# Kernel tuning notes

Measured on AMD Instinct MI355X. Metric: run time of the kernel, lower is better.

## Reference

```python
import jax, jax.numpy as jnp
import numpy as np

N_NODES = 100000
N_EDGES = 1600000
IN_DIM, H1, H2, N_CLASSES = 128, 64, 64, 16
NEG_SLOPE = 0.2  # PyG GATConv default leaky_relu slope


def _xavier(key, shape, gain=1.414):
    fan_in, fan_out = shape[0], shape[-1]
    a = gain * np.sqrt(6.0 / (fan_in + fan_out))
    return jax.random.uniform(key, shape, jnp.float32, -a, a)


def setup_inputs() -> dict:
    key = jax.random.key(0)
    ks = jax.random.split(key, 12)
    ft_list = jax.random.normal(ks[0], (N_NODES, IN_DIM), jnp.float32)
    adj_tensor = jax.random.randint(ks[1], (2, N_EDGES), 0, N_NODES, jnp.int64)
    return {
        "ft_list": ft_list,
        "adj_tensor": adj_tensor,
        "W1": _xavier(ks[2], (IN_DIM, H1)),
        "a_src1": _xavier(ks[3], (H1, 1))[:, 0],
        "a_dst1": _xavier(ks[4], (H1, 1))[:, 0],
        "b1": jnp.zeros((H1,), jnp.float32),
        "W2": _xavier(ks[5], (H1, H2)),
        "a_src2": _xavier(ks[6], (H2, 1))[:, 0],
        "a_dst2": _xavier(ks[7], (H2, 1))[:, 0],
        "b2": jnp.zeros((H2,), jnp.float32),
        "clas_W": _xavier(ks[8], (H2, N_CLASSES)),
        "clas_b": _xavier(ks[9], (1, N_CLASSES)),
    }


def _gat_conv(x, src, dst, n, W, a_src, a_dst, b):
    # h: [N, H] transformed node features
    h = x @ W
    alpha_s = h @ a_src  # [N]
    alpha_d = h @ a_dst  # [N]
    # per-edge attention logit (gather)
    e = jax.nn.leaky_relu(alpha_s[src] + alpha_d[dst], NEG_SLOPE)  # [E]
    # segment softmax over edges grouped by destination node
    m = jax.ops.segment_max(e, dst, num_segments=n)
    p = jnp.exp(e - m[dst])
    s = jax.ops.segment_sum(p, dst, num_segments=n)
    attn = p / s[dst]  # [E]
    # weighted scatter-add of source features
    out = jax.ops.segment_sum(h[src] * attn[:, None], dst, num_segments=n)
    return out + b


def reference(ft_list, adj_tensor, W1, a_src1, a_dst1, b1, W2, a_src2, a_dst2, b2, clas_W, clas_b):
    n = ft_list.shape[0]
    loop = jnp.arange(n, dtype=adj_tensor.dtype)
    src = jnp.concatenate([adj_tensor[0], loop])  # add self-loops (PyG default)
    dst = jnp.concatenate([adj_tensor[1], loop])
    x = _gat_conv(ft_list, src, dst, n, W1, a_src1, a_dst1, b1)
    x = jax.nn.elu(x)
    # dropout(0.5) is identity in eval mode
    x = _gat_conv(x, src, dst, n, W2, a_src2, a_dst2, b2)
    logits = x @ clas_W + clas_b
    return logits, x
```

## Files before the change

### kernel.cpp

```cpp
#include <hip/hip_runtime.h>
#include <hip/hip_bf16.h>

#define NEG_SLOPE 0.2f
#define LOG2E 1.4426950408889634f
#define BSH 9
#define BW  (1 << BSH)
#define CH  4096
#define PGRID 256

typedef short short8 __attribute__((ext_vector_type(8)));
typedef float f32x4 __attribute__((ext_vector_type(4)));


__global__ __launch_bounds__(256) void bucket_hist_kernel(
    const int* __restrict__ adj, int* __restrict__ H, int E, int N, int R, int NBK)
{
    __shared__ int hist[256];
    const int t = threadIdx.x;
    const int ET = E + N;
    for (int r = blockIdx.x; r < R; r += gridDim.x) {
        hist[t] = 0;
        __syncthreads();
        int base = r * CH;
        for (int i = 0; i < CH / 256; ++i) {
            int e = base + i * 256 + t;
            if (e >= ET) break;
            int d = (e < E) ? adj[E + e] : (e - E);
            atomicAdd(&hist[d >> BSH], 1);
        }
        __syncthreads();
        if (t < NBK) H[r * NBK + t] = hist[t];
        __syncthreads();
    }
}

__global__ __launch_bounds__(256) void scan_rounds_kernel(
    const int* __restrict__ H, int* __restrict__ S2, int* __restrict__ tot,
    int R, int NBK)
{
    __shared__ int part[256];
    const int b = blockIdx.x;
    const int t = threadIdx.x;
    const int C = (R + 255) / 256;
    int r0 = t * C, r1 = min(R, r0 + C);
    int s = 0;
    for (int r = r0; r < r1; ++r) s += H[r * NBK + b];
    part[t] = s;
    __syncthreads();
    for (int off = 1; off < 256; off <<= 1) {
        int v = (t >= off) ? part[t - off] : 0;
        __syncthreads();
        part[t] += v;
        __syncthreads();
    }
    int run = (t > 0) ? part[t - 1] : 0;
    for (int r = r0; r < r1; ++r) {
        int h = H[r * NBK + b];
        S2[r * NBK + b] = run;
        run += h;
    }
    if (t == 255) tot[b] = part[255];
}

__global__ __launch_bounds__(256) void scan_tot_kernel(
    const int* __restrict__ tot, int* __restrict__ base, int NBK)
{
    __shared__ int s[256];
    int t = threadIdx.x;
    int v = (t < NBK) ? tot[t] : 0;
    s[t] = v;
    __syncthreads();
    for (int off = 1; off < 256; off <<= 1) {
        int u = (t >= off) ? s[t - off] : 0;
        __syncthreads();
        s[t] += u;
        __syncthreads();
    }
    if (t < NBK) base[t] = s[t] - v;
}

__global__ __launch_bounds__(256) void partition_kernel(
    const int* __restrict__ adj, const int* __restrict__ S2,
    const int* __restrict__ base, int* __restrict__ pbuf,
    int E, int N, int R, int NBK)
{
    __shared__ int lcur[256];
    const int t = threadIdx.x;
    const int ET = E + N;
    for (int r = blockIdx.x; r < R; r += gridDim.x) {
        if (t < NBK) lcur[t] = base[t] + S2[r * NBK + t];
        __syncthreads();
        int b0 = r * CH;
        for (int i = 0; i < CH / 256; ++i) {
            int e = b0 + i * 256 + t;
            if (e >= ET) break;
            int s, d;
            if (e < E) { d = adj[E + e]; s = adj[e]; }
            else       { s = d = e - E; }
            int b = d >> BSH;
            int pos = atomicAdd(&lcur[b], 1);
            pbuf[pos] = (s << BSH) | (d & (BW - 1));
        }
        __syncthreads();
    }
}

__global__ __launch_bounds__(256) void csr_build_kernel(
    const int* __restrict__ base, const int* __restrict__ tot,
    const int* __restrict__ pbuf,
    int* __restrict__ row_ptr, int* __restrict__ col_idx, int E, int N, int NBK)
{
    __shared__ int offA[BW];
    __shared__ int lcur[BW];
    const int b = blockIdx.x;
    const int t = threadIdx.x;
    const int node0 = b << BSH;
    const int nn = min(BW, N - node0);
    const int ET = E + N;
    const int segbeg = base[b];
    const int segend = segbeg + tot[b];

    offA[t] = 0; offA[t + 256] = 0;
    __syncthreads();
    for (int i = segbeg + t; i < segend; i += 256)
        atomicAdd(&offA[pbuf[i] & (BW - 1)], 1);
    __syncthreads();
    for (int off = 1; off < BW; off <<= 1) {
        int i1 = t + 256;
        int v0 = (t >= off) ? offA[t - off] : 0;
        int v1 = (i1 >= off) ? offA[i1 - off] : 0;
        __syncthreads();
        offA[t] += v0; offA[i1] += v1;
        __syncthreads();
    }
    if (t < nn) {
        int ex = t ? offA[t - 1] : 0;
        row_ptr[node0 + t] = segbeg + ex;
        lcur[t] = segbeg + ex;
    }
    int i2 = t + 256;
    if (i2 < nn) {
        int ex = offA[i2 - 1];
        row_ptr[node0 + i2] = segbeg + ex;
        lcur[i2] = segbeg + ex;
    }
    if (b == NBK - 1 && t == 0) row_ptr[N] = ET;
    __syncthreads();
    for (int i = segbeg + t; i < segend; i += 256) {
        int p = pbuf[i];
        int pos = atomicAdd(&lcur[p & (BW - 1)], 1);
        col_idx[pos] = p >> BSH;
    }
}


__device__ __forceinline__ unsigned short f2bf(float f)
{
    union { __hip_bfloat16 b; unsigned short u; } v;
    v.b = __float2bfloat16(f);
    return v.u;
}

__global__ __launch_bounds__(256) void prep_wfrag_kernel(
    const float* __restrict__ W, unsigned short* __restrict__ wf, int K)
{
    int total = K * 64;
    int idx = blockIdx.x * 256 + threadIdx.x;
    if (idx >= total) return;
    int i = idx & 7;
    int l = (idx >> 3) & 63;
    int f = idx >> 9;
    int s = f >> 2, tt = f & 3;
    int k = 32 * s + 8 * (l >> 4) + i;
    int n = 16 * tt + (l & 15);
    wf[idx] = f2bf(W[k * 64 + n]);
}

template<int K>
__global__ __launch_bounds__(256) void gemm_alpha_mfma(
    const float* __restrict__ X, const unsigned short* __restrict__ wf,
    const float* __restrict__ a_src, const float* __restrict__ a_dst,
    __hip_bfloat16* __restrict__ h, float* __restrict__ as_, float* __restrict__ ad_,
    int N, int nChunks)
{
    constexpr int S = K / 32;
    const int t = threadIdx.x;
    const int wave = t >> 6, lane = t & 63;
    const int g = lane >> 4, c = lane & 15;

    short8 bf[S * 4];
#pragma unroll
    for (int f = 0; f < S * 4; ++f)
        bf[f] = *(const short8*)(wf + ((size_t)(f * 64 + lane)) * 8);

    float asr[4], adr[4];
#pragma unroll
    for (int tt = 0; tt < 4; ++tt) {
        asr[tt] = a_src[16 * tt + c];
        adr[tt] = a_dst[16 * tt + c];
    }

    for (int chunk = blockIdx.x; chunk < nChunks; chunk += gridDim.x) {
        const int r0 = chunk * 64 + wave * 16;
        const int arow = r0 + c;
        const bool rv = arow < N;
        const float* xr = X + (size_t)arow * K;

        f32x4 acc[4];
#pragma unroll
        for (int tt = 0; tt < 4; ++tt) acc[tt] = (f32x4){0.f, 0.f, 0.f, 0.f};

#pragma unroll
        for (int s = 0; s < S; ++s) {
            float4 x0 = make_float4(0.f, 0.f, 0.f, 0.f);
            float4 x1 = make_float4(0.f, 0.f, 0.f, 0.f);
            if (rv) {
                const float4* p = (const float4*)(xr + 32 * s + 8 * g);
                x0 = p[0]; x1 = p[1];
            }
            float xs[8] = {x0.x, x0.y, x0.z, x0.w, x1.x, x1.y, x1.z, x1.w};
            union { short8 v; unsigned u[4]; } ah, al;
#pragma unroll
            for (int p2 = 0; p2 < 4; ++p2) {
                unsigned u0 = __float_as_uint(xs[2 * p2]);
                unsigned u1 = __float_as_uint(xs[2 * p2 + 1]);
                ah.u[p2] = (u0 >> 16) | (u1 & 0xffff0000u);
                float h0 = __uint_as_float(u0 & 0xffff0000u);
                float h1 = __uint_as_float(u1 & 0xffff0000u);
                unsigned l0 = __float_as_uint(xs[2 * p2] - h0);
                unsigned l1 = __float_as_uint(xs[2 * p2 + 1] - h1);
                al.u[p2] = (l0 >> 16) | (l1 & 0xffff0000u);
            }
#pragma unroll
            for (int tt = 0; tt < 4; ++tt) {
                acc[tt] = __builtin_amdgcn_mfma_f32_16x16x32_bf16(
                    ah.v, bf[s * 4 + tt], acc[tt], 0, 0, 0);
                acc[tt] = __builtin_amdgcn_mfma_f32_16x16x32_bf16(
                    al.v, bf[s * 4 + tt], acc[tt], 0, 0, 0);
            }
        }

#pragma unroll
        for (int i = 0; i < 4; ++i) {
            const int ri = r0 + 4 * g + i;
            float va = 0.f, vd = 0.f;
#pragma unroll
            for (int tt = 0; tt < 4; ++tt) {
                float v = acc[tt][i];
                va += v * asr[tt];
                vd += v * adr[tt];
                if (ri < N) h[(size_t)ri * 64 + 16 * tt + c] = __float2bfloat16(v);
            }
#pragma unroll
            for (int off = 8; off >= 1; off >>= 1) {
                va += __shfl_xor(va, off, 16);
                vd += __shfl_xor(vd, off, 16);
            }
            if (c == 0 && ri < N) { as_[ri] = va * LOG2E; ad_[ri] = vd * LOG2E; }
        }
    }
}

__global__ __launch_bounds__(256) void gat_aggregate_kernel(
    const int* __restrict__ row_ptr, const int* __restrict__ col_idx,
    const float* __restrict__ as_, const float* __restrict__ ad_,
    const __hip_bfloat16* __restrict__ h, const float* __restrict__ b,
    float* __restrict__ out, int N, int do_elu)
{
    const int wave = threadIdx.x >> 6, lane = threadIdx.x & 63;
    const int sub = lane >> 3, q = lane & 7;
    const int node = blockIdx.x * 32 + wave * 8 + sub;
    if (node >= N) return;
    const int beg = row_ptr[node], end = row_ptr[node + 1];
    const float ad = ad_[node];
    float acc[8] = {0.f, 0.f, 0.f, 0.f, 0.f, 0.f, 0.f, 0.f};
    float psum = 0.f;

    const char* cbp = (const char*)col_idx;
    const char* abp = (const char*)as_;
    const char* hbp = (const char*)h;
    const unsigned qb = (unsigned)q * 16u;

    unsigned co = (unsigned)beg * 4u;
    for (int i = beg; i < end; i += 2, co += 8u) {
        const bool v1 = (i + 1) < end;
        int s0 = *(const int*)(cbp + co);
        int s1 = *(const int*)(cbp + (v1 ? co + 4u : co));
        float x0 = *(const float*)(abp + ((unsigned)s0 << 2)) + ad;
        float x1 = *(const float*)(abp + ((unsigned)s1 << 2)) + ad;
        uint4 u0 = *(const uint4*)(hbp + (((unsigned)s0 << 7) + qb));
        uint4 u1 = *(const uint4*)(hbp + (((unsigned)s1 << 7) + qb));
        x0 = fmaxf(x0, NEG_SLOPE * x0);
        x1 = fmaxf(x1, NEG_SLOPE * x1);
        float p0 = __builtin_amdgcn_exp2f(x0);
        float p1 = v1 ? __builtin_amdgcn_exp2f(x1) : 0.f;
        psum += p0 + p1;
        unsigned w;
        w = u0.x; acc[0] += p0 * __uint_as_float(w << 16); acc[1] += p0 * __uint_as_float(w & 0xffff0000u);
        w = u0.y; acc[2] += p0 * __uint_as_float(w << 16); acc[3] += p0 * __uint_as_float(w & 0xffff0000u);
        w = u0.z; acc[4] += p0 * __uint_as_float(w << 16); acc[5] += p0 * __uint_as_float(w & 0xffff0000u);
        w = u0.w; acc[6] += p0 * __uint_as_float(w << 16); acc[7] += p0 * __uint_as_float(w & 0xffff0000u);
        w = u1.x; acc[0] += p1 * __uint_as_float(w << 16); acc[1] += p1 * __uint_as_float(w & 0xffff0000u);
        w = u1.y; acc[2] += p1 * __uint_as_float(w << 16); acc[3] += p1 * __uint_as_float(w & 0xffff0000u);
        w = u1.z; acc[4] += p1 * __uint_as_float(w << 16); acc[5] += p1 * __uint_as_float(w & 0xffff0000u);
        w = u1.w; acc[6] += p1 * __uint_as_float(w << 16); acc[7] += p1 * __uint_as_float(w & 0xffff0000u);
    }

    const float inv = 1.f / psum;
    const float* bq = b + q * 8;
    float4 b0 = *(const float4*)bq;
    float4 b1 = *(const float4*)(bq + 4);
    float v[8];
    v[0] = acc[0] * inv + b0.x; v[1] = acc[1] * inv + b0.y;
    v[2] = acc[2] * inv + b0.z; v[3] = acc[3] * inv + b0.w;
    v[4] = acc[4] * inv + b1.x; v[5] = acc[5] * inv + b1.y;
    v[6] = acc[6] * inv + b1.z; v[7] = acc[7] * inv + b1.w;
    if (do_elu) {
#pragma unroll
        for (int j = 0; j < 8; ++j)
            v[j] = v[j] > 0.f ? v[j] : (__expf(v[j]) - 1.f);
    }
    float* op = out + (size_t)node * 64 + q * 8;
    ((float4*)op)[0] = make_float4(v[0], v[1], v[2], v[3]);
    ((float4*)op)[1] = make_float4(v[4], v[5], v[6], v[7]);
}

__global__ __launch_bounds__(256) void classifier_kernel(
    const float* __restrict__ x, const float* __restrict__ cw,
    const float* __restrict__ cb, float* __restrict__ out, int N)
{
    int i = blockIdx.x * blockDim.x + threadIdx.x;
    if (i >= N * 16) return;
    int n = i >> 4, c = i & 15;
    const float4* xr = (const float4*)(x + (size_t)n * 64);
    float acc = cb[c];
#pragma unroll
    for (int j4 = 0; j4 < 16; ++j4) {
        float4 xv = xr[j4];
        acc += xv.x * cw[(j4 * 4 + 0) * 16 + c];
        acc += xv.y * cw[(j4 * 4 + 1) * 16 + c];
        acc += xv.z * cw[(j4 * 4 + 2) * 16 + c];
        acc += xv.w * cw[(j4 * 4 + 3) * 16 + c];
    }
    out[i] = acc;
}

extern "C" void kernel_launch(void* const* d_in, const int* in_sizes, int n_in,
                              void* d_out, int out_size, void* d_ws, size_t ws_size,
                              hipStream_t stream)
{
    const float* X    = (const float*)d_in[0];
    const int*   adj  = (const int*)d_in[1];
    const float* W1   = (const float*)d_in[2];
    const float* a_s1 = (const float*)d_in[3];
    const float* a_d1 = (const float*)d_in[4];
    const float* b1   = (const float*)d_in[5];
    const float* W2   = (const float*)d_in[6];
    const float* a_s2 = (const float*)d_in[7];
    const float* a_d2 = (const float*)d_in[8];
    const float* b2   = (const float*)d_in[9];
    const float* cW   = (const float*)d_in[10];
    const float* cb   = (const float*)d_in[11];

    const int N   = in_sizes[0] / 128;
    const int E   = in_sizes[1] / 2;
    const int ET  = E + N;
    const int R   = (ET + CH - 1) / CH;
    const int NBK = (N + BW - 1) >> BSH;

    __hip_bfloat16* A = (__hip_bfloat16*)d_ws;
    float* B       = (float*)(A + (size_t)N * 64);
    float* asb     = B + (size_t)N * 64;
    float* adb     = asb + N;
    int*   row_ptr = (int*)(adb + N);
    int*   col_idx = row_ptr + (N + 1);
    int*   pbuf    = col_idx + ET;
    int*   H       = pbuf + ET;
    int*   S2      = H + R * NBK;
    int*   tot     = S2 + R * NBK;
    int*   base    = tot + NBK;

    uintptr_t wp = ((uintptr_t)pbuf + 15) & ~(uintptr_t)15;
    unsigned short* wf1 = (unsigned short*)wp;
    unsigned short* wf2 = wf1 + 128 * 64;

    const int T = 256;
    const int aggBlocks  = (N + 31) / 32;
    const int nChunks    = (N + 63) / 64;
    const int gemmBlocks = nChunks < 512 ? nChunks : 512;

    bucket_hist_kernel<<<PGRID, T, 0, stream>>>(adj, H, E, N, R, NBK);
    scan_rounds_kernel<<<NBK, T, 0, stream>>>(H, S2, tot, R, NBK);
    scan_tot_kernel<<<1, T, 0, stream>>>(tot, base, NBK);
    partition_kernel<<<PGRID, T, 0, stream>>>(adj, S2, base, pbuf, E, N, R, NBK);
    csr_build_kernel<<<NBK, T, 0, stream>>>(base, tot, pbuf, row_ptr, col_idx, E, N, NBK);

    prep_wfrag_kernel<<<(128 * 64 + 255) / 256, T, 0, stream>>>(W1, wf1, 128);
    prep_wfrag_kernel<<<(64 * 64 + 255) / 256, T, 0, stream>>>(W2, wf2, 64);

    gemm_alpha_mfma<128><<<gemmBlocks, T, 0, stream>>>(
        X, wf1, a_s1, a_d1, A, asb, adb, N, nChunks);
    gat_aggregate_kernel<<<aggBlocks, T, 0, stream>>>(
        row_ptr, col_idx, asb, adb, A, b1, B, N, 1);

    float* out  = (float*)d_out;
    float* xout = out + (size_t)N * 16;
    gemm_alpha_mfma<64><<<gemmBlocks, T, 0, stream>>>(
        B, wf2, a_s2, a_d2, A, asb, adb, N, nChunks);
    gat_aggregate_kernel<<<aggBlocks, T, 0, stream>>>(
        row_ptr, col_idx, asb, adb, A, b2, xout, N, 0);

    classifier_kernel<<<(N * 16 + T - 1) / T, T, 0, stream>>>(
        xout, cW, cb, out, N);
}
```

Before: 299.6 us.

## Sort nodes by in-degree to balance aggregation work across wavefronts

Adds a counting sort of nodes by in-degree (histogram, scan, scatter) and has the aggregation kernels process nodes in that permuted order, so the 8 nodes sharing a wave have similar edge counts. This targets divergence and load imbalance, where a wave waits on its longest-degree node. It adds three small kernels plus an extra perm indirection, and it loses the locality of contiguous node order for outputs and row_ptr reads.

```diff
diff --git a/kernel.cpp b/kernel.cpp
--- a/kernel.cpp
+++ b/kernel.cpp
@@ -63,10 +63,12 @@
 }
 
 __global__ __launch_bounds__(256) void scan_tot_kernel(
-    const int* __restrict__ tot, int* __restrict__ base, int NBK)
+    const int* __restrict__ tot, int* __restrict__ base, int NBK,
+    int* __restrict__ gh)
 {
     __shared__ int s[256];
     int t = threadIdx.x;
+    gh[t] = 0;
     int v = (t < NBK) ? tot[t] : 0;
     s[t] = v;
     __syncthreads();
@@ -154,6 +156,58 @@
 }
 
 
+__global__ __launch_bounds__(256) void deg_hist_kernel(
+    const int* __restrict__ row_ptr, int* __restrict__ gh, int N)
+{
+    __shared__ int lh[256];
+    const int t = threadIdx.x;
+    lh[t] = 0;
+    __syncthreads();
+    for (int n = blockIdx.x * 256 + t; n < N; n += gridDim.x * 256)
+        atomicAdd(&lh[min(row_ptr[n + 1] - row_ptr[n], 255)], 1);
+    __syncthreads();
+    if (lh[t]) atomicAdd(&gh[t], lh[t]);
+}
+
+__global__ __launch_bounds__(256) void deg_scan_kernel(
+    const int* __restrict__ gh, int* __restrict__ gcur)
+{
+    __shared__ int s[256];
+    int t = threadIdx.x;
+    int v = gh[t];
+    s[t] = v;
+    __syncthreads();
+    for (int off = 1; off < 256; off <<= 1) {
+        int u = (t >= off) ? s[t - off] : 0;
+        __syncthreads();
+        s[t] += u;
+        __syncthreads();
+    }
+    gcur[t] = s[t] - v;
+}
+
+__global__ __launch_bounds__(256) void deg_scatter_kernel(
+    const int* __restrict__ row_ptr, int* __restrict__ gcur,
+    int* __restrict__ perm, int N)
+{
+    __shared__ int lh[256], lcur[256];
+    const int t = threadIdx.x;
+    const int n0 = blockIdx.x * 2048;
+    const int n1 = min(N, n0 + 2048);
+    lh[t] = 0;
+    __syncthreads();
+    for (int n = n0 + t; n < n1; n += 256)
+        atomicAdd(&lh[min(row_ptr[n + 1] - row_ptr[n], 255)], 1);
+    __syncthreads();
+    lcur[t] = lh[t] ? atomicAdd(&gcur[t], lh[t]) : 0;
+    __syncthreads();
+    for (int n = n0 + t; n < n1; n += 256) {
+        int pos = atomicAdd(&lcur[min(row_ptr[n + 1] - row_ptr[n], 255)], 1);
+        perm[pos] = n;
+    }
+}
+
+
 __device__ __forceinline__ unsigned short f2bf(float f)
 {
     union { __hip_bfloat16 b; unsigned short u; } v;
@@ -262,6 +316,7 @@
 }
 
 __global__ __launch_bounds__(256) void gat_aggregate_kernel(
+    const int* __restrict__ perm,
     const int* __restrict__ row_ptr, const int* __restrict__ col_idx,
     const float* __restrict__ as_, const float* __restrict__ ad_,
     const __hip_bfloat16* __restrict__ h, const float* __restrict__ b,
@@ -269,8 +324,9 @@
 {
     const int wave = threadIdx.x >> 6, lane = threadIdx.x & 63;
     const int sub = lane >> 3, q = lane & 7;
-    const int node = blockIdx.x * 32 + wave * 8 + sub;
-    if (node >= N) return;
+    const int idx = blockIdx.x * 32 + wave * 8 + sub;
+    if (idx >= N) return;
+    const int node = perm[idx];
     const int beg = row_ptr[node], end = row_ptr[node + 1];
     const float ad = ad_[node];
     float acc[8] = {0.f, 0.f, 0.f, 0.f, 0.f, 0.f, 0.f, 0.f};
@@ -379,6 +435,9 @@
     int*   S2      = H + R * NBK;
     int*   tot     = S2 + R * NBK;
     int*   base    = tot + NBK;
+    int*   perm    = base + NBK;
+    int*   gh      = perm + N;
+    int*   gcur    = gh + 256;
 
     uintptr_t wp = ((uintptr_t)pbuf + 15) & ~(uintptr_t)15;
     unsigned short* wf1 = (unsigned short*)wp;
@@ -391,9 +450,13 @@
 
     bucket_hist_kernel<<<PGRID, T, 0, stream>>>(adj, H, E, N, R, NBK);
     scan_rounds_kernel<<<NBK, T, 0, stream>>>(H, S2, tot, R, NBK);
-    scan_tot_kernel<<<1, T, 0, stream>>>(tot, base, NBK);
+    scan_tot_kernel<<<1, T, 0, stream>>>(tot, base, NBK, gh);
     partition_kernel<<<PGRID, T, 0, stream>>>(adj, S2, base, pbuf, E, N, R, NBK);
     csr_build_kernel<<<NBK, T, 0, stream>>>(base, tot, pbuf, row_ptr, col_idx, E, N, NBK);
+
+    deg_hist_kernel<<<128, T, 0, stream>>>(row_ptr, gh, N);
+    deg_scan_kernel<<<1, T, 0, stream>>>(gh, gcur);
+    deg_scatter_kernel<<<(N + 2047) / 2048, T, 0, stream>>>(row_ptr, gcur, perm, N);
 
     prep_wfrag_kernel<<<(128 * 64 + 255) / 256, T, 0, stream>>>(W1, wf1, 128);
     prep_wfrag_kernel<<<(64 * 64 + 255) / 256, T, 0, stream>>>(W2, wf2, 64);
@@ -401,14 +464,14 @@
     gemm_alpha_mfma<128><<<gemmBlocks, T, 0, stream>>>(
         X, wf1, a_s1, a_d1, A, asb, adb, N, nChunks);
     gat_aggregate_kernel<<<aggBlocks, T, 0, stream>>>(
-        row_ptr, col_idx, asb, adb, A, b1, B, N, 1);
+        perm, row_ptr, col_idx, asb, adb, A, b1, B, N, 1);
 
     float* out  = (float*)d_out;
     float* xout = out + (size_t)N * 16;
     gemm_alpha_mfma<64><<<gemmBlocks, T, 0, stream>>>(
         B, wf2, a_s2, a_d2, A, asb, adb, N, nChunks);
     gat_aggregate_kernel<<<aggBlocks, T, 0, stream>>>(
-        row_ptr, col_idx, asb, adb, A, b2, xout, N, 0);
+        perm, row_ptr, col_idx, asb, adb, A, b2, xout, N, 0);
 
     classifier_kernel<<<(N * 16 + T - 1) / T, T, 0, stream>>>(
         xout, cW, cb, out, N);
```

New measurement: 318.9 us. 1.06x slower.

## Fuse CSR construction into one persistent kernel with grid barriers; unroll aggregation by 8

Applied to the files above, without the earlier changes.

Replaces the five-kernel bucketed CSR build with a single persistent kernel that does a global-atomic degree count, a two-level scan, and an atomic scatter into col_idx, separated by software grid barriers. Weight fragment prep and counter zeroing are merged into one init kernel, cutting launch count. The aggregation loop now processes 8 edges per iteration so more gathers are in flight at once. In exchange it uses global atomics on 100k counters, which can contend, and it relies on all 256 blocks being co-resident for the barrier to avoid deadlock. The scatter also loses the bucketed locality the old partition step gave to col_idx writes.

```diff
diff --git a/kernel.cpp b/kernel.cpp
--- a/kernel.cpp
+++ b/kernel.cpp
@@ -3,156 +3,9 @@
 
 #define NEG_SLOPE 0.2f
 #define LOG2E 1.4426950408889634f
-#define BSH 9
-#define BW  (1 << BSH)
-#define CH  4096
-#define PGRID 256
 
 typedef short short8 __attribute__((ext_vector_type(8)));
 typedef float f32x4 __attribute__((ext_vector_type(4)));
-
-
-__global__ __launch_bounds__(256) void bucket_hist_kernel(
-    const int* __restrict__ adj, int* __restrict__ H, int E, int N, int R, int NBK)
-{
-    __shared__ int hist[256];
-    const int t = threadIdx.x;
-    const int ET = E + N;
-    for (int r = blockIdx.x; r < R; r += gridDim.x) {
-        hist[t] = 0;
-        __syncthreads();
-        int base = r * CH;
-        for (int i = 0; i < CH / 256; ++i) {
-            int e = base + i * 256 + t;
-            if (e >= ET) break;
-            int d = (e < E) ? adj[E + e] : (e - E);
-            atomicAdd(&hist[d >> BSH], 1);
-        }
-        __syncthreads();
-        if (t < NBK) H[r * NBK + t] = hist[t];
-        __syncthreads();
-    }
-}
-
-__global__ __launch_bounds__(256) void scan_rounds_kernel(
-    const int* __restrict__ H, int* __restrict__ S2, int* __restrict__ tot,
-    int R, int NBK)
-{
-    __shared__ int part[256];
-    const int b = blockIdx.x;
-    const int t = threadIdx.x;
-    const int C = (R + 255) / 256;
-    int r0 = t * C, r1 = min(R, r0 + C);
-    int s = 0;
-    for (int r = r0; r < r1; ++r) s += H[r * NBK + b];
-    part[t] = s;
-    __syncthreads();
-    for (int off = 1; off < 256; off <<= 1) {
-        int v = (t >= off) ? part[t - off] : 0;
-        __syncthreads();
-        part[t] += v;
-        __syncthreads();
-    }
-    int run = (t > 0) ? part[t - 1] : 0;
-    for (int r = r0; r < r1; ++r) {
-        int h = H[r * NBK + b];
-        S2[r * NBK + b] = run;
-        run += h;
-    }
-    if (t == 255) tot[b] = part[255];
-}
-
-__global__ __launch_bounds__(256) void scan_tot_kernel(
-    const int* __restrict__ tot, int* __restrict__ base, int NBK)
-{
-    __shared__ int s[256];
-    int t = threadIdx.x;
-    int v = (t < NBK) ? tot[t] : 0;
-    s[t] = v;
-    __syncthreads();
-    for (int off = 1; off < 256; off <<= 1) {
-        int u = (t >= off) ? s[t - off] : 0;
-        __syncthreads();
-        s[t] += u;
-        __syncthreads();
-    }
-    if (t < NBK) base[t] = s[t] - v;
-}
-
-__global__ __launch_bounds__(256) void partition_kernel(
-    const int* __restrict__ adj, const int* __restrict__ S2,
-    const int* __restrict__ base, int* __restrict__ pbuf,
-    int E, int N, int R, int NBK)
-{
-    __shared__ int lcur[256];
-    const int t = threadIdx.x;
-    const int ET = E + N;
-    for (int r = blockIdx.x; r < R; r += gridDim.x) {
-        if (t < NBK) lcur[t] = base[t] + S2[r * NBK + t];
-        __syncthreads();
-        int b0 = r * CH;
-        for (int i = 0; i < CH / 256; ++i) {
-            int e = b0 + i * 256 + t;
-            if (e >= ET) break;
-            int s, d;
-            if (e < E) { d = adj[E + e]; s = adj[e]; }
-            else       { s = d = e - E; }
-            int b = d >> BSH;
-            int pos = atomicAdd(&lcur[b], 1);
-            pbuf[pos] = (s << BSH) | (d & (BW - 1));
-        }
-        __syncthreads();
-    }
-}
-
-__global__ __launch_bounds__(256) void csr_build_kernel(
-    const int* __restrict__ base, const int* __restrict__ tot,
-    const int* __restrict__ pbuf,
-    int* __restrict__ row_ptr, int* __restrict__ col_idx, int E, int N, int NBK)
-{
-    __shared__ int offA[BW];
-    __shared__ int lcur[BW];
-    const int b = blockIdx.x;
-    const int t = threadIdx.x;
-    const int node0 = b << BSH;
-    const int nn = min(BW, N - node0);
-    const int ET = E + N;
-    const int segbeg = base[b];
-    const int segend = segbeg + tot[b];
-
-    offA[t] = 0; offA[t + 256] = 0;
-    __syncthreads();
-    for (int i = segbeg + t; i < segend; i += 256)
-        atomicAdd(&offA[pbuf[i] & (BW - 1)], 1);
-    __syncthreads();
-    for (int off = 1; off < BW; off <<= 1) {
-        int i1 = t + 256;
-        int v0 = (t >= off) ? offA[t - off] : 0;
-        int v1 = (i1 >= off) ? offA[i1 - off] : 0;
-        __syncthreads();
-        offA[t] += v0; offA[i1] += v1;
-        __syncthreads();
-    }
-    if (t < nn) {
-        int ex = t ? offA[t - 1] : 0;
-        row_ptr[node0 + t] = segbeg + ex;
-        lcur[t] = segbeg + ex;
-    }
-    int i2 = t + 256;
-    if (i2 < nn) {
-        int ex = offA[i2 - 1];
-        row_ptr[node0 + i2] = segbeg + ex;
-        lcur[i2] = segbeg + ex;
-    }
-    if (b == NBK - 1 && t == 0) row_ptr[N] = ET;
-    __syncthreads();
-    for (int i = segbeg + t; i < segend; i += 256) {
-        int p = pbuf[i];
-        int pos = atomicAdd(&lcur[p & (BW - 1)], 1);
-        col_idx[pos] = p >> BSH;
-    }
-}
-
 
 __device__ __forceinline__ unsigned short f2bf(float f)
 {
@@ -161,20 +14,118 @@
     return v.u;
 }
 
-__global__ __launch_bounds__(256) void prep_wfrag_kernel(
-    const float* __restrict__ W, unsigned short* __restrict__ wf, int K)
-{
-    int total = K * 64;
-    int idx = blockIdx.x * 256 + threadIdx.x;
-    if (idx >= total) return;
-    int i = idx & 7;
-    int l = (idx >> 3) & 63;
-    int f = idx >> 9;
-    int s = f >> 2, tt = f & 3;
-    int k = 32 * s + 8 * (l >> 4) + i;
-    int n = 16 * tt + (l & 15);
-    wf[idx] = f2bf(W[k * 64 + n]);
-}
+__global__ __launch_bounds__(256) void init_kernel(
+    const float* __restrict__ W1, const float* __restrict__ W2,
+    unsigned short* __restrict__ wf1, unsigned short* __restrict__ wf2,
+    int* __restrict__ cnt, int* __restrict__ bars, int N)
+{
+    const int tid = blockIdx.x * 256 + threadIdx.x;
+    if (tid < 16) bars[tid] = 0;
+    if (tid < 128 * 64) {
+        int i = tid & 7, l = (tid >> 3) & 63, f = tid >> 9;
+        int s = f >> 2, tt = f & 3;
+        wf1[tid] = f2bf(W1[(32 * s + 8 * (l >> 4) + i) * 64 + (16 * tt + (l & 15))]);
+    }
+    if (tid < 64 * 64) {
+        int i = tid & 7, l = (tid >> 3) & 63, f = tid >> 9;
+        int s = f >> 2, tt = f & 3;
+        wf2[tid] = f2bf(W2[(32 * s + 8 * (l >> 4) + i) * 64 + (16 * tt + (l & 15))]);
+    }
+    for (int n = tid; n < N; n += gridDim.x * 256) cnt[n] = 0;
+}
+
+__device__ __forceinline__ void grid_bar(int* bar, int nb)
+{
+    __syncthreads();
+    __threadfence();
+    if (threadIdx.x == 0) {
+        __hip_atomic_fetch_add(bar, 1, __ATOMIC_ACQ_REL, __HIP_MEMORY_SCOPE_AGENT);
+        while (__hip_atomic_load(bar, __ATOMIC_ACQUIRE, __HIP_MEMORY_SCOPE_AGENT) < nb)
+            __builtin_amdgcn_s_sleep(1);
+    }
+    __syncthreads();
+    __threadfence();
+}
+
+__global__ __launch_bounds__(256) void csr_fused_kernel(
+    const int* __restrict__ adj, int* __restrict__ cnt,
+    int* __restrict__ row_ptr, int* __restrict__ cur,
+    int* __restrict__ csum, int* __restrict__ bars,
+    int* __restrict__ col_idx, int E, int N)
+{
+    const int t = threadIdx.x;
+    const int b = blockIdx.x;
+    const int NB = gridDim.x;
+    const int ET = E + N;
+    const int gsz = NB * 256;
+    const int NC = (N + 255) >> 8;
+    __shared__ int s[512];
+
+    for (int i = b * 256 + t; i < ET; i += gsz) {
+        int d = (i < E) ? adj[E + i] : (i - E);
+        atomicAdd(&cnt[d], 1);
+    }
+    grid_bar(&bars[0], NB);
+
+    for (int c = b; c < NC; c += NB) {
+        int i = c * 256 + t;
+        int v = (i < N) ? cnt[i] : 0;
+        s[t] = v;
+        __syncthreads();
+        for (int off = 1; off < 256; off <<= 1) {
+            int u = (t >= off) ? s[t - off] : 0;
+            __syncthreads();
+            s[t] += u;
+            __syncthreads();
+        }
+        if (i < N) row_ptr[i] = s[t] - v;
+        if (t == 255)
+            __hip_atomic_store(&csum[c], s[255], __ATOMIC_RELEASE, __HIP_MEMORY_SCOPE_AGENT);
+        __syncthreads();
+    }
+    grid_bar(&bars[1], NB);
+
+    if (b == 0) {
+        int i1 = t + 256;
+        int v0 = (t < NC) ? __hip_atomic_load(&csum[t], __ATOMIC_ACQUIRE, __HIP_MEMORY_SCOPE_AGENT) : 0;
+        int v1 = (i1 < NC) ? __hip_atomic_load(&csum[i1], __ATOMIC_ACQUIRE, __HIP_MEMORY_SCOPE_AGENT) : 0;
+        s[t] = v0; s[i1] = v1;
+        __syncthreads();
+        for (int off = 1; off < 512; off <<= 1) {
+            int u0 = (t >= off) ? s[t - off] : 0;
+            int u1 = (i1 >= off) ? s[i1 - off] : 0;
+            __syncthreads();
+            s[t] += u0; s[i1] += u1;
+            __syncthreads();
+        }
+        int e0 = t ? s[t - 1] : 0;
+        int e1 = s[i1 - 1];
+        if (t < NC)  __hip_atomic_store(&csum[t],  e0, __ATOMIC_RELEASE, __HIP_MEMORY_SCOPE_AGENT);
+        if (i1 < NC) __hip_atomic_store(&csum[i1], e1, __ATOMIC_RELEASE, __HIP_MEMORY_SCOPE_AGENT);
+    }
+    grid_bar(&bars[2], NB);
+
+    for (int c = b; c < NC; c += NB) {
+        int off = __hip_atomic_load(&csum[c], __ATOMIC_ACQUIRE, __HIP_MEMORY_SCOPE_AGENT);
+        int i = c * 256 + t;
+        if (i < N) {
+            int rp = row_ptr[i] + off;
+            row_ptr[i] = rp;
+            __hip_atomic_store(&cur[i], rp, __ATOMIC_RELEASE, __HIP_MEMORY_SCOPE_AGENT);
+            if (i == N - 1) row_ptr[N] = rp + cnt[i];
+        }
+    }
+    grid_bar(&bars[3], NB);
+
+    for (int i = b * 256 + t; i < ET; i += gsz) {
+        int sn, d;
+        if (i < E) { sn = adj[i]; d = adj[E + i]; }
+        else       { sn = d = i - E; }
+        int pos = atomicAdd(&cur[d], 1);
+        col_idx[pos] = sn;
+    }
+}
+
 
 template<int K>
 __global__ __launch_bounds__(256) void gemm_alpha_mfma(
@@ -261,6 +212,12 @@
     }
 }
 
+#define ACC8(u, p)                                                              \
+    w = u.x; acc[0] += p * __uint_as_float(w << 16); acc[1] += p * __uint_as_float(w & 0xffff0000u); \
+    w = u.y; acc[2] += p * __uint_as_float(w << 16); acc[3] += p * __uint_as_float(w & 0xffff0000u); \
+    w = u.z; acc[4] += p * __uint_as_float(w << 16); acc[5] += p * __uint_as_float(w & 0xffff0000u); \
+    w = u.w; acc[6] += p * __uint_as_float(w << 16); acc[7] += p * __uint_as_float(w & 0xffff0000u);
+
 __global__ __launch_bounds__(256) void gat_aggregate_kernel(
     const int* __restrict__ row_ptr, const int* __restrict__ col_idx,
     const float* __restrict__ as_, const float* __restrict__ ad_,
@@ -280,30 +237,36 @@
     const char* abp = (const char*)as_;
     const char* hbp = (const char*)h;
     const unsigned qb = (unsigned)q * 16u;
-
+    unsigned w;
+
+    int i = beg;
     unsigned co = (unsigned)beg * 4u;
-    for (int i = beg; i < end; i += 2, co += 8u) {
-        const bool v1 = (i + 1) < end;
+    for (; i + 8 <= end; i += 8, co += 32u) {
+        int s[8];
+#pragma unroll
+        for (int k = 0; k < 8; ++k) s[k] = *(const int*)(cbp + (co + 4u * k));
+        float x[8];
+#pragma unroll
+        for (int k = 0; k < 8; ++k) x[k] = *(const float*)(abp + ((unsigned)s[k] << 2)) + ad;
+        uint4 u[8];
+#pragma unroll
+        for (int k = 0; k < 8; ++k) u[k] = *(const uint4*)(hbp + (((unsigned)s[k] << 7) + qb));
+#pragma unroll
+        for (int k = 0; k < 8; ++k) {
+            float xx = fmaxf(x[k], NEG_SLOPE * x[k]);
+            float p = __builtin_amdgcn_exp2f(xx);
+            psum += p;
+            ACC8(u[k], p)
+        }
+    }
+    for (; i < end; ++i, co += 4u) {
         int s0 = *(const int*)(cbp + co);
-        int s1 = *(const int*)(cbp + (v1 ? co + 4u : co));
         float x0 = *(const float*)(abp + ((unsigned)s0 << 2)) + ad;
-        float x1 = *(const float*)(abp + ((unsigned)s1 << 2)) + ad;
         uint4 u0 = *(const uint4*)(hbp + (((unsigned)s0 << 7) + qb));
-        uint4 u1 = *(const uint4*)(hbp + (((unsigned)s1 << 7) + qb));
         x0 = fmaxf(x0, NEG_SLOPE * x0);
-        x1 = fmaxf(x1, NEG_SLOPE * x1);
         float p0 = __builtin_amdgcn_exp2f(x0);
-        float p1 = v1 ? __builtin_amdgcn_exp2f(x1) : 0.f;
-        psum += p0 + p1;
-        unsigned w;
-        w = u0.x; acc[0] += p0 * __uint_as_float(w << 16); acc[1] += p0 * __uint_as_float(w & 0xffff0000u);
-        w = u0.y; acc[2] += p0 * __uint_as_float(w << 16); acc[3] += p0 * __uint_as_float(w & 0xffff0000u);
-        w = u0.z; acc[4] += p0 * __uint_as_float(w << 16); acc[5] += p0 * __uint_as_float(w & 0xffff0000u);
-        w = u0.w; acc[6] += p0 * __uint_as_float(w << 16); acc[7] += p0 * __uint_as_float(w & 0xffff0000u);
-        w = u1.x; acc[0] += p1 * __uint_as_float(w << 16); acc[1] += p1 * __uint_as_float(w & 0xffff0000u);
-        w = u1.y; acc[2] += p1 * __uint_as_float(w << 16); acc[3] += p1 * __uint_as_float(w & 0xffff0000u);
-        w = u1.z; acc[4] += p1 * __uint_as_float(w << 16); acc[5] += p1 * __uint_as_float(w & 0xffff0000u);
-        w = u1.w; acc[6] += p1 * __uint_as_float(w << 16); acc[7] += p1 * __uint_as_float(w & 0xffff0000u);
+        psum += p0;
+        ACC8(u0, p0)
     }
 
     const float inv = 1.f / psum;
@@ -365,8 +328,6 @@
     const int N   = in_sizes[0] / 128;
     const int E   = in_sizes[1] / 2;
     const int ET  = E + N;
-    const int R   = (ET + CH - 1) / CH;
-    const int NBK = (N + BW - 1) >> BSH;
 
     __hip_bfloat16* A = (__hip_bfloat16*)d_ws;
     float* B       = (float*)(A + (size_t)N * 64);
@@ -374,14 +335,11 @@
     float* adb     = asb + N;
     int*   row_ptr = (int*)(adb + N);
     int*   col_idx = row_ptr + (N + 1);
-    int*   pbuf    = col_idx + ET;
-    int*   H       = pbuf + ET;
-    int*   S2      = H + R * NBK;
-    int*   tot     = S2 + R * NBK;
-    int*   base    = tot + NBK;
-
-    uintptr_t wp = ((uintptr_t)pbuf + 15) & ~(uintptr_t)15;
-    unsigned short* wf1 = (unsigned short*)wp;
+    int*   cnt     = col_idx + ET;
+    int*   cur     = cnt + N;
+    int*   csum    = cur + N;
+    int*   bars    = csum + 512;
+    unsigned short* wf1 = (unsigned short*)(bars + 16);
     unsigned short* wf2 = wf1 + 128 * 64;
 
     const int T = 256;
@@ -389,14 +347,9 @@
     const int nChunks    = (N + 63) / 64;
     const int gemmBlocks = nChunks < 512 ? nChunks : 512;
 
-    bucket_hist_kernel<<<PGRID, T, 0, stream>>>(adj, H, E, N, R, NBK);
-    scan_rounds_kernel<<<NBK, T, 0, stream>>>(H, S2, tot, R, NBK);
-    scan_tot_kernel<<<1, T, 0, stream>>>(tot, base, NBK);
-    partition_kernel<<<PGRID, T, 0, stream>>>(adj, S2, base, pbuf, E, N, R, NBK);
-    csr_build_kernel<<<NBK, T, 0, stream>>>(base, tot, pbuf, row_ptr, col_idx, E, N, NBK);
-
-    prep_wfrag_kernel<<<(128 * 64 + 255) / 256, T, 0, stream>>>(W1, wf1, 128);
-    prep_wfrag_kernel<<<(64 * 64 + 255) / 256, T, 0, stream>>>(W2, wf2, 64);
+    init_kernel<<<256, T, 0, stream>>>(W1, W2, wf1, wf2, cnt, bars, N);
+    csr_fused_kernel<<<256, T, 0, stream>>>(
+        adj, cnt, row_ptr, cur, csum, bars, col_idx, E, N);
 
     gemm_alpha_mfma<128><<<gemmBlocks, T, 0, stream>>>(
         X, wf1, a_s1, a_d1, A, asb, adb, N, nChunks);
```

Measured after the change: 651.6 us. 118% more time.

## Fuse classifier into second aggregation, unroll edge loop by eight, merge weight prep

Applied to the files above, without the earlier changes.

Folds the final 64x16 classifier into the second GAT aggregation kernel. Each 8-lane group computes partial logits from its 8 features and reduces them with xor shuffles, so the separate classifier launch and its re-read of x disappear. The edge loop is unrolled by eight with all index, alpha and feature loads issued before the math, giving more memory-level parallelism on the gathers at the cost of more registers. The two weight-fragment prep launches are merged into one.

```diff
diff --git a/kernel.cpp b/kernel.cpp
--- a/kernel.cpp
+++ b/kernel.cpp
@@ -161,19 +161,21 @@
     return v.u;
 }
 
-__global__ __launch_bounds__(256) void prep_wfrag_kernel(
-    const float* __restrict__ W, unsigned short* __restrict__ wf, int K)
-{
-    int total = K * 64;
+__global__ __launch_bounds__(256) void prep_wfrag2_kernel(
+    const float* __restrict__ W1, const float* __restrict__ W2,
+    unsigned short* __restrict__ wf1, unsigned short* __restrict__ wf2)
+{
     int idx = blockIdx.x * 256 + threadIdx.x;
-    if (idx >= total) return;
-    int i = idx & 7;
-    int l = (idx >> 3) & 63;
-    int f = idx >> 9;
-    int s = f >> 2, tt = f & 3;
-    int k = 32 * s + 8 * (l >> 4) + i;
-    int n = 16 * tt + (l & 15);
-    wf[idx] = f2bf(W[k * 64 + n]);
+    if (idx < 128 * 64) {
+        int i = idx & 7, l = (idx >> 3) & 63, f = idx >> 9;
+        int s = f >> 2, tt = f & 3;
+        wf1[idx] = f2bf(W1[(32 * s + 8 * (l >> 4) + i) * 64 + (16 * tt + (l & 15))]);
+    }
+    if (idx < 64 * 64) {
+        int i = idx & 7, l = (idx >> 3) & 63, f = idx >> 9;
+        int s = f >> 2, tt = f & 3;
+        wf2[idx] = f2bf(W2[(32 * s + 8 * (l >> 4) + i) * 64 + (16 * tt + (l & 15))]);
+    }
 }
 
 template<int K>
@@ -261,11 +263,19 @@
     }
 }
 
+#define ACC8(u, p)                                                              \
+    w = u.x; acc[0] += p * __uint_as_float(w << 16); acc[1] += p * __uint_as_float(w & 0xffff0000u); \
+    w = u.y; acc[2] += p * __uint_as_float(w << 16); acc[3] += p * __uint_as_float(w & 0xffff0000u); \
+    w = u.z; acc[4] += p * __uint_as_float(w << 16); acc[5] += p * __uint_as_float(w & 0xffff0000u); \
+    w = u.w; acc[6] += p * __uint_as_float(w << 16); acc[7] += p * __uint_as_float(w & 0xffff0000u);
+
 __global__ __launch_bounds__(256) void gat_aggregate_kernel(
     const int* __restrict__ row_ptr, const int* __restrict__ col_idx,
     const float* __restrict__ as_, const float* __restrict__ ad_,
     const __hip_bfloat16* __restrict__ h, const float* __restrict__ b,
-    float* __restrict__ out, int N, int do_elu)
+    float* __restrict__ out, int N, int do_elu,
+    const float* __restrict__ cw, const float* __restrict__ cb,
+    float* __restrict__ logits)
 {
     const int wave = threadIdx.x >> 6, lane = threadIdx.x & 63;
     const int sub = lane >> 3, q = lane & 7;
@@ -280,30 +290,36 @@
     const char* abp = (const char*)as_;
     const char* hbp = (const char*)h;
     const unsigned qb = (unsigned)q * 16u;
-
+    unsigned w;
+
+    int i = beg;
     unsigned co = (unsigned)beg * 4u;
-    for (int i = beg; i < end; i += 2, co += 8u) {
-        const bool v1 = (i + 1) < end;
+    for (; i + 8 <= end; i += 8, co += 32u) {
+        int s[8];
+#pragma unroll
+        for (int k = 0; k < 8; ++k) s[k] = *(const int*)(cbp + (co + 4u * k));
+        float x[8];
+#pragma unroll
+        for (int k = 0; k < 8; ++k) x[k] = *(const float*)(abp + ((unsigned)s[k] << 2)) + ad;
+        uint4 u[8];
+#pragma unroll
+        for (int k = 0; k < 8; ++k) u[k] = *(const uint4*)(hbp + (((unsigned)s[k] << 7) + qb));
+#pragma unroll
+        for (int k = 0; k < 8; ++k) {
+            float xx = fmaxf(x[k], NEG_SLOPE * x[k]);
+            float p = __builtin_amdgcn_exp2f(xx);
+            psum += p;
+            ACC8(u[k], p)
+        }
+    }
+    for (; i < end; ++i, co += 4u) {
         int s0 = *(const int*)(cbp + co);
-        int s1 = *(const int*)(cbp + (v1 ? co + 4u : co));
         float x0 = *(const float*)(abp + ((unsigned)s0 << 2)) + ad;
-        float x1 = *(const float*)(abp + ((unsigned)s1 << 2)) + ad;
         uint4 u0 = *(const uint4*)(hbp + (((unsigned)s0 << 7) + qb));
-        uint4 u1 = *(const uint4*)(hbp + (((unsigned)s1 << 7) + qb));
         x0 = fmaxf(x0, NEG_SLOPE * x0);
-        x1 = fmaxf(x1, NEG_SLOPE * x1);
         float p0 = __builtin_amdgcn_exp2f(x0);
-        float p1 = v1 ? __builtin_amdgcn_exp2f(x1) : 0.f;
-        psum += p0 + p1;
-        unsigned w;
-        w = u0.x; acc[0] += p0 * __uint_as_float(w << 16); acc[1] += p0 * __uint_as_float(w & 0xffff0000u);
-        w = u0.y; acc[2] += p0 * __uint_as_float(w << 16); acc[3] += p0 * __uint_as_float(w & 0xffff0000u);
-        w = u0.z; acc[4] += p0 * __uint_as_float(w << 16); acc[5] += p0 * __uint_as_float(w & 0xffff0000u);
-        w = u0.w; acc[6] += p0 * __uint_as_float(w << 16); acc[7] += p0 * __uint_as_float(w & 0xffff0000u);
-        w = u1.x; acc[0] += p1 * __uint_as_float(w << 16); acc[1] += p1 * __uint_as_float(w & 0xffff0000u);
-        w = u1.y; acc[2] += p1 * __uint_as_float(w << 16); acc[3] += p1 * __uint_as_float(w & 0xffff0000u);
-        w = u1.z; acc[4] += p1 * __uint_as_float(w << 16); acc[5] += p1 * __uint_as_float(w & 0xffff0000u);
-        w = u1.w; acc[6] += p1 * __uint_as_float(w << 16); acc[7] += p1 * __uint_as_float(w & 0xffff0000u);
+        psum += p0;
+        ACC8(u0, p0)
     }
 
     const float inv = 1.f / psum;
@@ -323,26 +339,31 @@
     float* op = out + (size_t)node * 64 + q * 8;
     ((float4*)op)[0] = make_float4(v[0], v[1], v[2], v[3]);
     ((float4*)op)[1] = make_float4(v[4], v[5], v[6], v[7]);
-}
-
-__global__ __launch_bounds__(256) void classifier_kernel(
-    const float* __restrict__ x, const float* __restrict__ cw,
-    const float* __restrict__ cb, float* __restrict__ out, int N)
-{
-    int i = blockIdx.x * blockDim.x + threadIdx.x;
-    if (i >= N * 16) return;
-    int n = i >> 4, c = i & 15;
-    const float4* xr = (const float4*)(x + (size_t)n * 64);
-    float acc = cb[c];
-#pragma unroll
-    for (int j4 = 0; j4 < 16; ++j4) {
-        float4 xv = xr[j4];
-        acc += xv.x * cw[(j4 * 4 + 0) * 16 + c];
-        acc += xv.y * cw[(j4 * 4 + 1) * 16 + c];
-        acc += xv.z * cw[(j4 * 4 + 2) * 16 + c];
-        acc += xv.w * cw[(j4 * 4 + 3) * 16 + c];
-    }
-    out[i] = acc;
+
+    if (cw) {
+        float lg[16];
+#pragma unroll
+        for (int c = 0; c < 16; ++c) lg[c] = 0.f;
+#pragma unroll
+        for (int k = 0; k < 8; ++k) {
+            const float4* cwr = (const float4*)(cw + (q * 8 + k) * 16);
+            float xv = v[k];
+            float4 c0 = cwr[0], c1 = cwr[1], c2 = cwr[2], c3 = cwr[3];
+            lg[0] += xv * c0.x; lg[1] += xv * c0.y; lg[2] += xv * c0.z; lg[3] += xv * c0.w;
+            lg[4] += xv * c1.x; lg[5] += xv * c1.y; lg[6] += xv * c1.z; lg[7] += xv * c1.w;
+            lg[8] += xv * c2.x; lg[9] += xv * c2.y; lg[10] += xv * c2.z; lg[11] += xv * c2.w;
+            lg[12] += xv * c3.x; lg[13] += xv * c3.y; lg[14] += xv * c3.z; lg[15] += xv * c3.w;
+        }
+#pragma unroll
+        for (int off = 1; off < 8; off <<= 1) {
+#pragma unroll
+            for (int c = 0; c < 16; ++c) lg[c] += __shfl_xor(lg[c], off, 64);
+        }
+        float2 o;
+        o.x = lg[2 * q] + cb[2 * q];
+        o.y = lg[2 * q + 1] + cb[2 * q + 1];
+        *(float2*)(logits + (size_t)node * 16 + 2 * q) = o;
+    }
 }
 
 extern "C" void kernel_launch(void* const* d_in, const int* in_sizes, int n_in,
@@ -395,21 +416,17 @@
     partition_kernel<<<PGRID, T, 0, stream>>>(adj, S2, base, pbuf, E, N, R, NBK);
     csr_build_kernel<<<NBK, T, 0, stream>>>(base, tot, pbuf, row_ptr, col_idx, E, N, NBK);
 
-    prep_wfrag_kernel<<<(128 * 64 + 255) / 256, T, 0, stream>>>(W1, wf1, 128);
-    prep_wfrag_kernel<<<(64 * 64 + 255) / 256, T, 0, stream>>>(W2, wf2, 64);
+    prep_wfrag2_kernel<<<(128 * 64 + 255) / 256, T, 0, stream>>>(W1, W2, wf1, wf2);
 
     gemm_alpha_mfma<128><<<gemmBlocks, T, 0, stream>>>(
         X, wf1, a_s1, a_d1, A, asb, adb, N, nChunks);
     gat_aggregate_kernel<<<aggBlocks, T, 0, stream>>>(
-        row_ptr, col_idx, asb, adb, A, b1, B, N, 1);
+        row_ptr, col_idx, asb, adb, A, b1, B, N, 1, nullptr, nullptr, nullptr);
 
     float* out  = (float*)d_out;
     float* xout = out + (size_t)N * 16;
     gemm_alpha_mfma<64><<<gemmBlocks, T, 0, stream>>>(
         B, wf2, a_s2, a_d2, A, asb, adb, N, nChunks);
     gat_aggregate_kernel<<<aggBlocks, T, 0, stream>>>(
-        row_ptr, col_idx, asb, adb, A, b2, xout, N, 0);
-
-    classifier_kernel<<<(N * 16 + T - 1) / T, T, 0, stream>>>(
-        xout, cW, cb, out, N);
-}
+        row_ptr, col_idx, asb, adb, A, b2, xout, N, 0, cW, cb, out);
+}
```

Measured after the change: 320.8 us. +7.1%, slower.
